# Performance work log

Hardware: AMD Instinct MI355X
Metric: run time of the kernel (lower is better)

The kernel has to match this reference:

```python
import jax, jax.numpy as jnp
import numpy as np

N_NODES = 100000
N_EDGES = 3200000
D_FEAT = 64
K_HOPS = 3


def setup_inputs() -> dict:
    key = jax.random.key(0)
    k1, k2, k3, k4 = jax.random.split(key, 4)
    x = jax.random.normal(k1, (N_NODES, D_FEAT), dtype=jnp.float32)
    edge_weight = jax.random.uniform(k2, (N_EDGES,), dtype=jnp.float32)
    src = jax.random.randint(k3, (N_EDGES,), 0, N_NODES, dtype=jnp.int32)
    dst = jax.random.randint(k4, (N_EDGES,), 0, N_NODES, dtype=jnp.int32)
    return {"x": x, "edge_weight": edge_weight, "src": src, "dst": dst}


def reference(x, edge_weight, src, dst):
    # k-hop weighted SpMM: h <- scatter_sum(h[src] * w, dst), repeated K_HOPS times.
    # Dropouts are identity in eval mode (rates set to 0.0).
    h = x
    for _ in range(K_HOPS):
        msg = h[src] * edge_weight[:, None]          # [E, d] gather-multiply
        h = jax.ops.segment_sum(msg, dst, num_segments=N_NODES)  # [N, d] scatter-sum
    return h
```

## Files before the change

### kernel.cpp

```cpp
#include <hip/hip_runtime.h>

#define D_FEAT 64
#define CHUNK 4096
#define BSHIFT 9
#define BSIZE 512
#define NPW 8

typedef unsigned int uint;
typedef unsigned short ushort;
typedef unsigned char uchar;

static __device__ __forceinline__ ushort f2bf(float f) {
    uint u = __float_as_uint(f);
    uint r = (u + 0x7fffu + ((u >> 16) & 1u)) >> 16;
    return (ushort)r;
}
static __device__ __forceinline__ float bf2f(ushort b) {
    return __uint_as_float(((uint)b) << 16);
}
static __device__ __forceinline__ float wq2f(uint ev) {
    return (float)(ev & 32767u) * (1.0f / 32768.0f) + (1.0f / 65536.0f);
}

__global__ void bucket_hist(const int* __restrict__ dst, int* __restrict__ bcount, int n_edges) {
    __shared__ int h[256];
    h[threadIdx.x] = 0;
    __syncthreads();
    for (int e = blockIdx.x * blockDim.x + threadIdx.x; e < n_edges; e += gridDim.x * blockDim.x)
        atomicAdd(&h[dst[e] >> BSHIFT], 1);
    __syncthreads();
    int v = h[threadIdx.x];
    if (v) atomicAdd(&bcount[threadIdx.x], v);
}

__global__ void bucket_scan(const int* __restrict__ bcount, int* __restrict__ bbase,
                            int* __restrict__ bcursor) {
    __shared__ int s[256];
    int t = threadIdx.x;
    int v = bcount[t];
    s[t] = v;
    __syncthreads();
    for (int off = 1; off < 256; off <<= 1) {
        int u = (t >= off) ? s[t - off] : 0;
        __syncthreads();
        s[t] += u;
        __syncthreads();
    }
    int excl = s[t] - v;
    bbase[t] = excl;
    bcursor[t] = excl;
}

__global__ __launch_bounds__(256) void partition_kernel(
        const int* __restrict__ src, const int* __restrict__ dst,
        const float* __restrict__ w, int* __restrict__ bcursor,
        int2* __restrict__ inter, int n_edges) {
    __shared__ int hist[256];
    __shared__ int lofs[256];
    __shared__ int cur[256];
    __shared__ int gbase[256];
    __shared__ int2 buf[CHUNK];
    __shared__ uchar bb[CHUNK];
    int t = threadIdx.x;
    int beg = blockIdx.x * CHUNK;
    int end = min(beg + CHUNK, n_edges);
    int cnt = end - beg;

    hist[t] = 0;
    __syncthreads();
    for (int i = beg + t; i < end; i += 256)
        atomicAdd(&hist[dst[i] >> BSHIFT], 1);
    __syncthreads();
    int v = hist[t];
    lofs[t] = v;
    __syncthreads();
    for (int off = 1; off < 256; off <<= 1) {
        int u = (t >= off) ? lofs[t - off] : 0;
        __syncthreads();
        lofs[t] += u;
        __syncthreads();
    }
    int excl = lofs[t] - v;
    __syncthreads();
    lofs[t] = excl;
    cur[t]  = excl;
    __syncthreads();
    for (int i = beg + t; i < end; i += 256) {
        int d = dst[i];
        int b = d >> BSHIFT;
        int p = atomicAdd(&cur[b], 1);
        buf[p] = make_int2((src[i] << BSHIFT) | (d & (BSIZE - 1)), __float_as_int(w[i]));
        bb[p] = (uchar)b;
    }
    __syncthreads();
    if (hist[t]) gbase[t] = atomicAdd(&bcursor[t], hist[t]);
    __syncthreads();
    for (int i = t; i < cnt; i += 256) {
        int b = bb[i];
        inter[gbase[b] + (i - lofs[b])] = buf[i];
    }
}

__global__ __launch_bounds__(512) void finalize_kernel(
        const int2* __restrict__ inter, const int* __restrict__ bbase,
        const int* __restrict__ bcount, uint* __restrict__ edges,
        int* __restrict__ row_ptr, int n_nodes, int n_edges) {
    __shared__ int hist[BSIZE];
    __shared__ int cur[BSIZE];
    int b = blockIdx.x;
    int t = threadIdx.x;
    int base = bbase[b];
    int cnt  = bcount[b];

    hist[t] = 0;
    __syncthreads();
    for (int i = t; i < cnt; i += BSIZE)
        atomicAdd(&hist[inter[base + i].x & (BSIZE - 1)], 1);
    __syncthreads();
    int v = hist[t];
    cur[t] = v;
    __syncthreads();
    for (int off = 1; off < BSIZE; off <<= 1) {
        int u = (t >= off) ? cur[t - off] : 0;
        __syncthreads();
        cur[t] += u;
        __syncthreads();
    }
    int excl = cur[t] - v;
    int node = (b << BSHIFT) + t;
    if (node < n_nodes) row_ptr[node] = base + excl;
    if (b == 0 && t == 0) row_ptr[n_nodes] = n_edges;
    __syncthreads();
    cur[t] = excl;
    __syncthreads();
    for (int i = t; i < cnt; i += BSIZE) {
        int2 r = inter[base + i];
        int dlo = r.x & (BSIZE - 1);
        int p = atomicAdd(&cur[dlo], 1);
        float wf = __int_as_float(r.y);
        uint wq = (uint)(wf * 32768.0f);
        if (wq > 32767u) wq = 32767u;
        edges[base + p] = ((uint)(r.x >> BSHIFT) << 15) | wq;
    }
}

__global__ void cvt_bf16(const float* __restrict__ in, ushort* __restrict__ out, int n4) {
    int i = blockIdx.x * blockDim.x + threadIdx.x;
    int stride = gridDim.x * blockDim.x;
    for (; i < n4; i += stride) {
        float4 v = ((const float4*)in)[i];
        ushort4 o;
        o.x = f2bf(v.x); o.y = f2bf(v.y); o.z = f2bf(v.z); o.w = f2bf(v.w);
        ((ushort4*)out)[i] = o;
    }
}

template <bool OUT_BF16>
__global__ __launch_bounds__(256) void gather_hop(
        const ushort* __restrict__ h, const uint* __restrict__ edges,
        const int* __restrict__ row_ptr, void* __restrict__ out_v, int n_nodes) {
    int wv = blockIdx.x * 4 + (threadIdx.x >> 6);
    int n0 = __builtin_amdgcn_readfirstlane(wv * NPW);
    if (n0 >= n_nodes) return;
    int f = threadIdx.x & 63;

    int rp[NPW + 1];
    #pragma unroll
    for (int i = 0; i <= NPW; ++i)
        rp[i] = row_ptr[min(n0 + i, n_nodes)];

    #pragma unroll
    for (int ni = 0; ni < NPW; ++ni) {
        int node = n0 + ni;
        if (node >= n_nodes) break;
        int beg = __builtin_amdgcn_readfirstlane(rp[ni]);
        int end = __builtin_amdgcn_readfirstlane(rp[ni + 1]);
        float acc = 0.0f;
        int j = beg;
        for (; j + 8 <= end; j += 8) {
            #pragma unroll
            for (int k = 0; k < 8; ++k) {
                uint ev = edges[j + k];
                acc += wq2f(ev) * bf2f(h[((size_t)(ev >> 15) << 6) + f]);
            }
        }
        for (; j < end; ++j) {
            uint ev = edges[j];
            acc += wq2f(ev) * bf2f(h[((size_t)(ev >> 15) << 6) + f]);
        }
        size_t o = ((size_t)node << 6) + f;
        if (OUT_BF16) ((ushort*)out_v)[o] = f2bf(acc);
        else          ((float*)out_v)[o]  = acc;
    }
}

extern "C" void kernel_launch(void* const* d_in, const int* in_sizes, int n_in,
                              void* d_out, int out_size, void* d_ws, size_t ws_size,
                              hipStream_t stream) {
    const float* x   = (const float*)d_in[0];
    const float* ew  = (const float*)d_in[1];
    const int*   src = (const int*)d_in[2];
    const int*   dst = (const int*)d_in[3];
    float* out = (float*)d_out;

    const int n_nodes = in_sizes[0] / D_FEAT;
    const int n_edges = in_sizes[1];
    const int nbuck   = (n_nodes + BSIZE - 1) >> BSHIFT;
    const int n_feat_total = n_nodes * D_FEAT;

    const size_t ed8_bytes = (size_t)n_edges * 8;
    const size_t ed4_bytes = (size_t)n_edges * 4;
    const size_t bf_bytes  = (size_t)n_feat_total * 2;

    char* ws = (char*)d_ws;
    int2*   inter  = (int2*)ws;
    ushort* x_bf   = (ushort*)ws;
    ushort* buf1   = (ushort*)(ws + bf_bytes);
    ws += (ed8_bytes > 2 * bf_bytes ? ed8_bytes : 2 * bf_bytes);
    uint* edges    = (uint*)ws;                 ws += ed4_bytes;
    int*  row_ptr  = (int*)ws;                  ws += (size_t)(n_nodes + 1) * 4;
    int*  bcount   = (int*)ws;                  ws += 256 * 4;
    int*  bbase    = (int*)ws;                  ws += 256 * 4;
    int*  bcursor  = (int*)ws;

    hipMemsetAsync(bcount, 0, 256 * 4, stream);
    bucket_hist<<<512, 256, 0, stream>>>(dst, bcount, n_edges);
    bucket_scan<<<1, 256, 0, stream>>>(bcount, bbase, bcursor);
    partition_kernel<<<(n_edges + CHUNK - 1) / CHUNK, 256, 0, stream>>>(
        src, dst, ew, bcursor, inter, n_edges);
    finalize_kernel<<<nbuck, BSIZE, 0, stream>>>(
        inter, bbase, bcount, edges, row_ptr, n_nodes, n_edges);

    cvt_bf16<<<1024, 256, 0, stream>>>(x, x_bf, n_feat_total / 4);

    const int waves = (n_nodes + NPW - 1) / NPW;
    const int grd = (waves + 3) / 4;
    gather_hop<true ><<<grd, 256, 0, stream>>>(x_bf, edges, row_ptr, buf1, n_nodes);
    gather_hop<true ><<<grd, 256, 0, stream>>>(buf1, edges, row_ptr, x_bf, n_nodes);
    gather_hop<false><<<grd, 256, 0, stream>>>(x_bf, edges, row_ptr, out,  n_nodes);
}
```

Measured before the change: 315.0 us.

## Shrink partition intermediates, fold bucket scan into consumers, vectorize histogram

The separate bucket_scan launch is removed, and each partition and finalize block now recomputes the bucket prefix sum from bcount. The intermediate edge record shrinks from 8 bytes to 6: a packed src/quantized-weight word plus a 16-bit local destination. Weight quantization moves into the partition pass. The histogram reads dst as int4, CHUNK doubles to 8192, and the middle hop uses 16 nodes per wave. The aim is less intermediate traffic and one fewer launch, at the cost of redundant per-block scans and more shared memory per partition block, which may lower occupancy.

```diff
diff --git a/kernel.cpp b/kernel.cpp
--- a/kernel.cpp
+++ b/kernel.cpp
@@ -1,10 +1,9 @@
 #include <hip/hip_runtime.h>
 
 #define D_FEAT 64
-#define CHUNK 4096
+#define CHUNK 8192
 #define BSHIFT 9
 #define BSIZE 512
-#define NPW 8
 
 typedef unsigned int uint;
 typedef unsigned short ushort;
@@ -26,41 +25,36 @@
     __shared__ int h[256];
     h[threadIdx.x] = 0;
     __syncthreads();
-    for (int e = blockIdx.x * blockDim.x + threadIdx.x; e < n_edges; e += gridDim.x * blockDim.x)
-        atomicAdd(&h[dst[e] >> BSHIFT], 1);
+    int tid = blockIdx.x * blockDim.x + threadIdx.x;
+    int stride = gridDim.x * blockDim.x;
+    int n4 = n_edges >> 2;
+    for (int i = tid; i < n4; i += stride) {
+        int4 d = ((const int4*)dst)[i];
+        atomicAdd(&h[d.x >> BSHIFT], 1);
+        atomicAdd(&h[d.y >> BSHIFT], 1);
+        atomicAdd(&h[d.z >> BSHIFT], 1);
+        atomicAdd(&h[d.w >> BSHIFT], 1);
+    }
+    for (int i = (n4 << 2) + tid; i < n_edges; i += stride)
+        atomicAdd(&h[dst[i] >> BSHIFT], 1);
     __syncthreads();
     int v = h[threadIdx.x];
     if (v) atomicAdd(&bcount[threadIdx.x], v);
 }
 
-__global__ void bucket_scan(const int* __restrict__ bcount, int* __restrict__ bbase,
-                            int* __restrict__ bcursor) {
-    __shared__ int s[256];
-    int t = threadIdx.x;
-    int v = bcount[t];
-    s[t] = v;
-    __syncthreads();
-    for (int off = 1; off < 256; off <<= 1) {
-        int u = (t >= off) ? s[t - off] : 0;
-        __syncthreads();
-        s[t] += u;
-        __syncthreads();
-    }
-    int excl = s[t] - v;
-    bbase[t] = excl;
-    bcursor[t] = excl;
-}
-
 __global__ __launch_bounds__(256) void partition_kernel(
         const int* __restrict__ src, const int* __restrict__ dst,
-        const float* __restrict__ w, int* __restrict__ bcursor,
-        int2* __restrict__ inter, int n_edges) {
+        const float* __restrict__ w, const int* __restrict__ bcount,
+        int* __restrict__ bcursor,
+        uint* __restrict__ interp, ushort* __restrict__ interd, int n_edges) {
     __shared__ int hist[256];
     __shared__ int lofs[256];
     __shared__ int cur[256];
     __shared__ int gbase[256];
-    __shared__ int2 buf[CHUNK];
-    __shared__ uchar bb[CHUNK];
+    __shared__ int scn[256];
+    __shared__ uint   bufp[CHUNK];
+    __shared__ ushort bufd[CHUNK];
+    __shared__ uchar  bb[CHUNK];
     int t = threadIdx.x;
     int beg = blockIdx.x * CHUNK;
     int end = min(beg + CHUNK, n_edges);
@@ -72,16 +66,15 @@
         atomicAdd(&hist[dst[i] >> BSHIFT], 1);
     __syncthreads();
     int v = hist[t];
-    lofs[t] = v;
+    scn[t] = v;
     __syncthreads();
     for (int off = 1; off < 256; off <<= 1) {
-        int u = (t >= off) ? lofs[t - off] : 0;
-        __syncthreads();
-        lofs[t] += u;
-        __syncthreads();
-    }
-    int excl = lofs[t] - v;
-    __syncthreads();
+        int u = (t >= off) ? scn[t - off] : 0;
+        __syncthreads();
+        scn[t] += u;
+        __syncthreads();
+    }
+    int excl = scn[t] - v;
     lofs[t] = excl;
     cur[t]  = excl;
     __syncthreads();
@@ -89,33 +82,59 @@
         int d = dst[i];
         int b = d >> BSHIFT;
         int p = atomicAdd(&cur[b], 1);
-        buf[p] = make_int2((src[i] << BSHIFT) | (d & (BSIZE - 1)), __float_as_int(w[i]));
-        bb[p] = (uchar)b;
-    }
-    __syncthreads();
-    if (hist[t]) gbase[t] = atomicAdd(&bcursor[t], hist[t]);
+        float wf = w[i];
+        uint wq = (uint)(wf * 32768.0f);
+        if (wq > 32767u) wq = 32767u;
+        bufp[p] = ((uint)src[i] << 15) | wq;
+        bufd[p] = (ushort)(d & (BSIZE - 1));
+        bb[p]   = (uchar)b;
+    }
+    __syncthreads();
+    int bcv = bcount[t];
+    scn[t] = bcv;
+    __syncthreads();
+    for (int off = 1; off < 256; off <<= 1) {
+        int u = (t >= off) ? scn[t - off] : 0;
+        __syncthreads();
+        scn[t] += u;
+        __syncthreads();
+    }
+    int gbb = scn[t] - bcv;
+    if (hist[t]) gbase[t] = gbb + atomicAdd(&bcursor[t], hist[t]);
     __syncthreads();
     for (int i = t; i < cnt; i += 256) {
         int b = bb[i];
-        inter[gbase[b] + (i - lofs[b])] = buf[i];
+        int pos = gbase[b] + (i - lofs[b]);
+        interp[pos] = bufp[i];
+        interd[pos] = bufd[i];
     }
 }
 
 __global__ __launch_bounds__(512) void finalize_kernel(
-        const int2* __restrict__ inter, const int* __restrict__ bbase,
+        const uint* __restrict__ interp, const ushort* __restrict__ interd,
         const int* __restrict__ bcount, uint* __restrict__ edges,
         int* __restrict__ row_ptr, int n_nodes, int n_edges) {
     __shared__ int hist[BSIZE];
     __shared__ int cur[BSIZE];
+    __shared__ int scn[256];
     int b = blockIdx.x;
     int t = threadIdx.x;
-    int base = bbase[b];
-    int cnt  = bcount[b];
+
+    if (t < 256) scn[t] = bcount[t];
+    __syncthreads();
+    for (int off = 1; off < 256; off <<= 1) {
+        int u = (t < 256 && t >= off) ? scn[t - off] : 0;
+        __syncthreads();
+        if (t < 256) scn[t] += u;
+        __syncthreads();
+    }
+    int base = (b == 0) ? 0 : scn[b - 1];
+    int cnt  = scn[b] - base;
 
     hist[t] = 0;
     __syncthreads();
     for (int i = t; i < cnt; i += BSIZE)
-        atomicAdd(&hist[inter[base + i].x & (BSIZE - 1)], 1);
+        atomicAdd(&hist[interd[base + i]], 1);
     __syncthreads();
     int v = hist[t];
     cur[t] = v;
@@ -134,13 +153,9 @@
     cur[t] = excl;
     __syncthreads();
     for (int i = t; i < cnt; i += BSIZE) {
-        int2 r = inter[base + i];
-        int dlo = r.x & (BSIZE - 1);
+        int dlo = interd[base + i];
         int p = atomicAdd(&cur[dlo], 1);
-        float wf = __int_as_float(r.y);
-        uint wq = (uint)(wf * 32768.0f);
-        if (wq > 32767u) wq = 32767u;
-        edges[base + p] = ((uint)(r.x >> BSHIFT) << 15) | wq;
+        edges[base + p] = interp[base + i];
     }
 }
 
@@ -155,22 +170,22 @@
     }
 }
 
-template <bool OUT_BF16>
+template <int NPWT, bool OUT_BF16>
 __global__ __launch_bounds__(256) void gather_hop(
         const ushort* __restrict__ h, const uint* __restrict__ edges,
         const int* __restrict__ row_ptr, void* __restrict__ out_v, int n_nodes) {
     int wv = blockIdx.x * 4 + (threadIdx.x >> 6);
-    int n0 = __builtin_amdgcn_readfirstlane(wv * NPW);
+    int n0 = __builtin_amdgcn_readfirstlane(wv * NPWT);
     if (n0 >= n_nodes) return;
     int f = threadIdx.x & 63;
 
-    int rp[NPW + 1];
+    int rp[NPWT + 1];
     #pragma unroll
-    for (int i = 0; i <= NPW; ++i)
+    for (int i = 0; i <= NPWT; ++i)
         rp[i] = row_ptr[min(n0 + i, n_nodes)];
 
     #pragma unroll
-    for (int ni = 0; ni < NPW; ++ni) {
+    for (int ni = 0; ni < NPWT; ++ni) {
         int node = n0 + ni;
         if (node >= n_nodes) break;
         int beg = __builtin_amdgcn_readfirstlane(rp[ni]);
@@ -208,34 +223,33 @@
     const int nbuck   = (n_nodes + BSIZE - 1) >> BSHIFT;
     const int n_feat_total = n_nodes * D_FEAT;
 
-    const size_t ed8_bytes = (size_t)n_edges * 8;
     const size_t ed4_bytes = (size_t)n_edges * 4;
+    const size_t ed2_bytes = (size_t)n_edges * 2;
     const size_t bf_bytes  = (size_t)n_feat_total * 2;
 
-    char* ws = (char*)d_ws;
-    int2*   inter  = (int2*)ws;
-    ushort* x_bf   = (ushort*)ws;
-    ushort* buf1   = (ushort*)(ws + bf_bytes);
-    ws += (ed8_bytes > 2 * bf_bytes ? ed8_bytes : 2 * bf_bytes);
-    uint* edges    = (uint*)ws;                 ws += ed4_bytes;
-    int*  row_ptr  = (int*)ws;                  ws += (size_t)(n_nodes + 1) * 4;
-    int*  bcount   = (int*)ws;                  ws += 256 * 4;
-    int*  bbase    = (int*)ws;                  ws += 256 * 4;
-    int*  bcursor  = (int*)ws;
-
-    hipMemsetAsync(bcount, 0, 256 * 4, stream);
+    char* wp = (char*)d_ws;
+    uint*   interp = (uint*)wp;
+    ushort* interd = (ushort*)(wp + ed4_bytes);
+    ushort* x_bf   = (ushort*)wp;
+    ushort* buf1   = (ushort*)(wp + bf_bytes);
+    wp += 2 * bf_bytes;
+    uint* edges    = (uint*)wp;                  wp += ed4_bytes;
+    int*  row_ptr  = (int*)wp;                   wp += (size_t)(n_nodes + 1) * 4;
+    int*  bcount   = (int*)wp;                   wp += 256 * 4;
+    int*  bcursor  = (int*)wp;
+
+    hipMemsetAsync(bcount, 0, 512 * 4, stream);
     bucket_hist<<<512, 256, 0, stream>>>(dst, bcount, n_edges);
-    bucket_scan<<<1, 256, 0, stream>>>(bcount, bbase, bcursor);
     partition_kernel<<<(n_edges + CHUNK - 1) / CHUNK, 256, 0, stream>>>(
-        src, dst, ew, bcursor, inter, n_edges);
+        src, dst, ew, bcount, bcursor, interp, interd, n_edges);
     finalize_kernel<<<nbuck, BSIZE, 0, stream>>>(
-        inter, bbase, bcount, edges, row_ptr, n_nodes, n_edges);
+        interp, interd, bcount, edges, row_ptr, n_nodes, n_edges);
 
     cvt_bf16<<<1024, 256, 0, stream>>>(x, x_bf, n_feat_total / 4);
 
-    const int waves = (n_nodes + NPW - 1) / NPW;
-    const int grd = (waves + 3) / 4;
-    gather_hop<true ><<<grd, 256, 0, stream>>>(x_bf, edges, row_ptr, buf1, n_nodes);
-    gather_hop<true ><<<grd, 256, 0, stream>>>(buf1, edges, row_ptr, x_bf, n_nodes);
-    gather_hop<false><<<grd, 256, 0, stream>>>(x_bf, edges, row_ptr, out,  n_nodes);
-}
+    const int grd8  = ((n_nodes + 8 * 4 - 1) / (8 * 4));
+    const int grd16 = ((n_nodes + 16 * 4 - 1) / (16 * 4));
+    gather_hop< 8, true ><<<grd8,  256, 0, stream>>>(x_bf, edges, row_ptr, buf1, n_nodes);
+    gather_hop<16, true ><<<grd16, 256, 0, stream>>>(buf1, edges, row_ptr, x_bf, n_nodes);
+    gather_hop< 8, false><<<grd8,  256, 0, stream>>>(x_bf, edges, row_ptr, out,  n_nodes);
+}
```

Measured after the change: 354.7 us. +12.6%, slower.
